# Optimization experiments

Hardware: AMD Instinct MI355X
Metric: run time of the kernel (lower is better)

The kernel has to match this reference:

```python
import jax, jax.numpy as jnp
import numpy as np

B, S, T, H, E, V = 64, 128, 64, 512, 256, 10000


def setup_inputs() -> dict:
    key = jax.random.key(0)
    ks = jax.random.split(key, 16)
    w = 0.05
    return {
        "trg": jax.random.randint(ks[0], (B, T), 0, V),
        "encoder_hidden": jax.random.normal(ks[1], (B, S, 2 * H), jnp.float32),
        "src_lengths": jax.random.randint(ks[2], (B,), 1, S + 1),
        "h0": jax.random.normal(ks[3], (B, H), jnp.float32),
        "c0": jax.random.normal(ks[4], (B, H), jnp.float32),
        "emb_table": jax.random.normal(ks[5], (V, E), jnp.float32) * w,
        "Wkey": jax.random.normal(ks[6], (2 * H, H), jnp.float32) * w,      # attention.key_layer
        "Wquery": jax.random.normal(ks[7], (H, H), jnp.float32) * w,        # attention.query_layer
        "we": jax.random.normal(ks[8], (H,), jnp.float32) * w,              # attention.energy_layer
        "W_ih": jax.random.normal(ks[9], (4 * H, E + 2 * H), jnp.float32) * w,
        "W_hh": jax.random.normal(ks[10], (4 * H, H), jnp.float32) * w,
        "b_ih": jnp.zeros((4 * H,), jnp.float32),
        "b_hh": jnp.zeros((4 * H,), jnp.float32),
        "Wpre": jax.random.normal(ks[11], (3 * H + E, H), jnp.float32) * w,  # pre_output_layer (no bias)
        "Wgen": jax.random.normal(ks[12], (H, V), jnp.float32) * w,          # generator / softmax head
    }


def reference(trg, encoder_hidden, src_lengths, h0, c0, emb_table, Wkey, Wquery,
              we, W_ih, W_hh, b_ih, b_hh, Wpre, Wgen):
    # Teacher-forced unroll (teacher_forcing=True branch); dropout in eval mode.
    s = encoder_hidden.shape[1]
    proj_key = encoder_hidden @ Wkey                            # [B,S,H]
    mask = jnp.arange(s)[None, :] < src_lengths[:, None]        # [B,S]
    embs = emb_table[trg]                                       # [B,T,E]

    def step(carry, emb_t):
        h, c = carry                                            # [B,H] each
        q = h @ Wquery                                          # query = last-layer hidden
        e = jnp.einsum('bsh,h->bs', jnp.tanh(q[:, None, :] + proj_key), we)
        a = jax.nn.softmax(jnp.where(mask, e, -1e9), axis=-1)   # masked attention
        ctx = jnp.einsum('bs,bsd->bd', a, encoder_hidden)       # [B,2H]
        x = jnp.concatenate([emb_t, ctx], axis=-1)              # rnn_input
        g = x @ W_ih.T + h @ W_hh.T + b_ih + b_hh
        i_g, f_g, g_g, o_g = jnp.split(g, 4, axis=-1)           # torch LSTM gate order
        c_new = jax.nn.sigmoid(f_g) * c + jax.nn.sigmoid(i_g) * jnp.tanh(g_g)
        h_new = jax.nn.sigmoid(o_g) * jnp.tanh(c_new)
        pre = jnp.concatenate([emb_t, h_new, ctx], axis=-1) @ Wpre
        logp = jax.nn.log_softmax(pre @ Wgen, axis=-1)          # [B,V]
        return (h_new, c_new), logp

    (hf, cf), out = jax.lax.scan(step, (h0, c0), jnp.swapaxes(embs, 0, 1))
    return jnp.transpose(out, (1, 2, 0)), hf, cf                # out: [B,V,T]
```

## Files before the change

### kernel.cpp

```cpp
#include <hip/hip_runtime.h>

#define B 64
#define S 128
#define T 64
#define H 512
#define E 256
#define V 10000
#define H2 1024
#define G4 2048
#define KX 1536
#define KP 1792
#define VP 10112
#define NROW 4096

typedef unsigned short u16;
typedef __attribute__((ext_vector_type(8))) short bf16x8;
typedef __attribute__((ext_vector_type(4))) short bf16x4;
typedef __attribute__((ext_vector_type(4))) float floatx4;

__device__ inline float b2f(u16 h){
  union { unsigned int u; float f; } v; v.u = ((unsigned int)h) << 16; return v.f;
}
__device__ inline u16 f2b(float f){
  union { unsigned int u; float f; } v; v.f = f;
// ... 156 lines not shown
    *(bf16x8*)&sA[ar*32 + ((ch ^ swz)*8)] = pa;
    #pragma unroll
    for (int i=0;i<NB;i++)
      *(bf16x8*)&sB[(i*64+ar)*32 + ((ch ^ swz)*8)] = pb[i];
    __syncthreads();
    if (k0 + 32 < K){
      pa = *(const bf16x8*)(gA + k0 + 32);
      #pragma unroll
      for (int i=0;i<NB;i++) pb[i] = *(const bf16x8*)(BT + (size_t)(n0+i*64+ar)*ldb + k0+32 + ch*8);
    }
    bf16x8 af = *(const bf16x8*)&sA[(16*wv + (lane&15))*32 + (((lane>>4) ^ px)*8)];
    #pragma unroll
    for (int s=0;s<NSUB;s++){
      bf16x8 bfv = *(const bf16x8*)&sB[(16*s + (lane&15))*32 + (((lane>>4) ^ px)*8)];
      acc[s] = __builtin_amdgcn_mfma_f32_16x16x32_bf16(af, bfv, acc[s], 0, 0, 0);
    }
  }

  if constexpr (EPI == 0 || EPI == 4){
    #pragma unroll
    for (int s=0;s<NSUB;s++)
      #pragma unroll
      for (int r=0;r<4;r++){
        int row = row0 + 16*wv + ((lane>>4)<<2) + r;
        int col = n0 + 16*s + (lane&15);
        if (EPI == 4) row = ((row & 63) << 6) | (row >> 6);
        outb[(size_t)row*ldc + col] = f2b(acc[s][r]);
      }
  }
  if constexpr (EPI == 2){
    float sr[4] = {0.f,0.f,0.f,0.f};
    #pragma unroll
    for (int s=0;s<NSUB;s++){
      int col = n0 + 16*s + (lane&15);
      if (col < V){
        #pragma unroll
        for (int r=0;r<4;r++) sr[r] += __expf(acc[s][r]);
      }
    }
    #pragma unroll
    for (int r=0;r<4;r++){
      float v = sr[r];
      v += __shfl_xor(v,1); v += __shfl_xor(v,2); v += __shfl_xor(v,4); v += __shfl_xor(v,8);
      sr[r] = v;
    }
    if ((lane&15)==0){
      #pragma unroll
      for (int r=0;r<4;r++){
        int row = row0 + 16*wv + ((lane>>4)<<2) + r;
        sep[(size_t)row*80 + blockIdx.y] = sr[r];
      }
    }
  }
  if constexpr (EPI == 3){
    #pragma unroll
    for (int s=0;s<NSUB;s++)
      #pragma unroll
      for (int r=0;r<4;r++){
        int rl = 16*wv + ((lane>>4)<<2) + r;
        int cl = 16*s + (lane&15);
        Cx[cl*65 + rl] = acc[s][r];
      }
    if (tid < 64) lseb[tid] = lse[row0 + tid];
    __syncthreads();
    int b = blockIdx.x;
    for (int idx = tid; idx < TN*16; idx += 256){
      int vl = idx >> 4, q4 = idx & 15;
      int v = n0 + vl;
      if (v < V){
        floatx4 o;
        o[0] = Cx[vl*65 + q4*4+0] - lseb[q4*4+0];
        o[1] = Cx[vl*65 + q4*4+1] - lseb[q4*4+1];
        o[2] = Cx[vl*65 + q4*4+2] - lseb[q4*4+2];
        o[3] = Cx[vl*65 + q4*4+3] - lseb[q4*4+3];
        *(floatx4*)&outp[((size_t)b*V + v)*T + q4*4] = o;
      }
    }
  }
}

__device__ __forceinline__ void wait_flags(unsigned* base, unsigned g){
  if (threadIdx.x < 64){
    unsigned* p = base + (unsigned)threadIdx.x*64;
    int it = 0;
    while (ld_if(p) < g && ++it < 5000000) asm volatile("s_sleep 1":::);
  }
  __syncthreads();
}

__global__ __launch_bounds__(512) void decoder_loop(
    u16* __restrict__ xgs, const float* __restrict__ c0f, float* __restrict__ outp,
    const u16* __restrict__ pk, const u16* __restrict__ encbT,
    const float* __restrict__ we, const int* __restrict__ lens,
    const u16* __restrict__ wqT, u16* __restrict__ cph,
    const u16* __restrict__ wch, const u16* __restrict__ gembt,
    const float* __restrict__ bias, unsigned* __restrict__ bar)
{
  __shared__ u16 sA[64*128];
  __shared__ u16 sB[32*128];
  __shared__ float Cx[64*36];
  __shared__ __align__(16) u16 hsb[H];
  __shared__ __align__(16) float qw[H];
  __shared__ __align__(16) float wel[H];
  __shared__ float ep[512];
  __shared__ float ev[S];
  __shared__ __align__(16) u16 alb[S];
  __shared__ __align__(16) float ctxf[H2];
  __shared__ float smax, sinv;

  const int tid = threadIdx.x, lane = tid & 63, wv = tid >> 6;
  const int blk = blockIdx.x;
  const int b = blk;
  const int lenb = lens[b];
  unsigned* flag_ctx = bar;
  unsigned* flag_h   = bar + 64*64;

  const int n0 = blk*32;
  const int kh = wv >> 2, wr = wv & 3;
  const int rs0 = tid >> 4, gs = tid & 15;
  const int rowa = 16*wr + (lane & 15);
  const int pb_ = tid >> 3, jl = tid & 7;
  const int jglob = n0/4 + jl;
  float creg = c0f[pb_*H + jglob];
  floatx4 bias4 = *(const floatx4*)(bias + n0 + jl*4);

  wel[tid] = we[tid];
  __syncthreads();

  for (int t=0; t<T; t++){
    u16* xgt = xgs + (size_t)t*B*KX;
    u16* xgn = xgs + (size_t)(t+1)*B*KX;

    wait_flags(flag_h, (unsigned)t);
    hsb[tid] = xgt[b*KX + H2 + tid];
    __syncthreads();

    {
      floatx4 accq[4];
      #pragma unroll
      for (int s=0;s<4;s++) accq[s] = (floatx4){0.f,0.f,0.f,0.f};
      const int kc = (lane>>4)*8;
      #pragma unroll 4
      for (int ks=0; ks<16; ks++){
        bf16x8 af = *(const bf16x8*)&hsb[ks*32 + kc];
        #pragma unroll
        for (int s=0;s<4;s++){
          const u16* bp = wqT + (size_t)(wv*64 + s*16 + (lane&15))*H + ks*32 + kc;
          accq[s] = __builtin_amdgcn_mfma_f32_16x16x32_bf16(af, *(const bf16x8*)bp, accq[s], 0, 0, 0);
        }
      }
      if (lane < 16){
        #pragma unroll
        for (int s=0;s<4;s++) qw[wv*64 + s*16 + lane] = accq[s][0];
      }
    }
    __syncthreads();

    {
      int s = tid >> 2, part = tid & 3;
      float a0 = 0.f;
      if (s < lenb){
        const u16* pr = pk + (size_t)(b*S + s)*H;
        #pragma unroll 4
        for (int m=0;m<16;m++){
          int k0 = part*8 + m*32;
          bf16x8 p8 = *(const bf16x8*)(pr + k0);
          floatx4 qa = *(const floatx4*)&qw[k0];
          floatx4 qb = *(const floatx4*)&qw[k0+4];
          floatx4 wa = *(const floatx4*)&wel[k0];
          floatx4 wb = *(const floatx4*)&wel[k0+4];
          #pragma unroll
          for (int i=0;i<4;i++){
            a0 += tanh_fast(qa[i] + b2f((u16)p8[i]))   * wa[i];
            a0 += tanh_fast(qb[i] + b2f((u16)p8[i+4])) * wb[i];
          }
        }
      }
      ep[tid] = a0;
    }
    __syncthreads();
    if (tid < S){
      float e = ep[tid*4] + ep[tid*4+1] + ep[tid*4+2] + ep[tid*4+3];
      ev[tid] = (tid < lenb) ? e : -1e30f;
    }
    __syncthreads();
    if (tid < 64){
      float m = fmaxf(ev[tid], ev[tid+64]);
      #pragma unroll
      for (int o=32;o>=1;o>>=1) m = fmaxf(m, __shfl_xor(m,o));
      if (tid==0) smax = m;
    }
    __syncthreads();
    if (tid < S) ev[tid] = __expf(ev[tid]-smax);
    __syncthreads();
    if (tid < 64){
      float s2 = ev[tid] + ev[tid+64];
      #pragma unroll
      for (int o=32;o>=1;o>>=1) s2 += __shfl_xor(s2,o);
      if (tid==0) sinv = rcpf(s2);
    }
    __syncthreads();
    if (tid < S) alb[tid] = f2b(ev[tid]*sinv);
    __syncthreads();

    {
      floatx4 accc[8];
      #pragma unroll
      for (int s=0;s<8;s++) accc[s] = (floatx4){0.f,0.f,0.f,0.f};
      const int kc = (lane>>4)*8;
      #pragma unroll
      for (int ks=0; ks<4; ks++){
        bf16x8 af = *(const bf16x8*)&alb[ks*32 + kc];
        #pragma unroll
        for (int s8=0;s8<8;s8++){
          const u16* bp = encbT + ((size_t)b*H2 + wv*128 + s8*16 + (lane&15))*S + ks*32 + kc;
          accc[s8] = __builtin_amdgcn_mfma_f32_16x16x32_bf16(af, *(const bf16x8*)bp, accc[s8], 0, 0, 0);
        }
      }
      if (lane < 16){
        #pragma unroll
        for (int s8=0;s8<8;s8++) ctxf[wv*128 + s8*16 + lane] = accc[s8][0];
      }
    }
    __syncthreads();
    {
      int d = tid*2;
      unsigned pack = ((unsigned)f2b(ctxf[d+1]) << 16) | (unsigned)f2b(ctxf[d]);
      st_wt_u32(xgt + (size_t)b*KX + d, pack);
      *(unsigned*)&cph[(size_t)(b*T + t)*KP + E + H + d] = pack;
    }
    asm volatile("s_waitcnt vmcnt(0)" ::: "memory");
    __syncthreads();
    if (tid == 0) st_if(flag_ctx + (unsigned)b*64, (unsigned)(t+1));

    floatx4 gacc[2];
    gacc[0] = (floatx4){0.f,0.f,0.f,0.f};
    gacc[1] = (floatx4){0.f,0.f,0.f,0.f};
    {
      bf16x8 a0 = *(const bf16x8*)(xgt + (size_t)rs0*KX + 1024 + gs*8);
      bf16x8 a1 = *(const bf16x8*)(xgt + (size_t)(rs0+32)*KX + 1024 + gs*8);
      bf16x8 b0 = *(const bf16x8*)(wch + (size_t)(n0+rs0)*KX + 1024 + gs*8);
      for (int kk=8; kk<12; kk++){
        __syncthreads();
        *(bf16x8*)&sA[rs0*128 + ((gs ^ (rs0&7))*8)] = a0;
        *(bf16x8*)&sA[(rs0+32)*128 + ((gs ^ (rs0&7))*8)] = a1;
        *(bf16x8*)&sB[rs0*128 + ((gs ^ (rs0&7))*8)] = b0;
        __syncthreads();
        if (kk < 11){
          int ko = (kk+1)*128;
          a0 = *(const bf16x8*)(xgt + (size_t)rs0*KX + ko + gs*8);
          a1 = *(const bf16x8*)(xgt + (size_t)(rs0+32)*KX + ko + gs*8);
          b0 = *(const bf16x8*)(wch + (size_t)(n0+rs0)*KX + ko + gs*8);
        }
        #pragma unroll
        for (int ks=0; ks<2; ks++){
          int gq = kh*8 + ks*4 + (lane>>4);
          bf16x8 af = *(const bf16x8*)&sA[rowa*128 + ((gq ^ (rowa&7))*8)];
          #pragma unroll
          for (int s=0;s<2;s++){
            int rowb = 16*s + (lane & 15);
            bf16x8 bfv = *(const bf16x8*)&sB[rowb*128 + ((gq ^ (rowb&7))*8)];
            gacc[s] = __builtin_amdgcn_mfma_f32_16x16x32_bf16(af, bfv, gacc[s], 0, 0, 0);
          }
        }
      }
    }

    wait_flags(flag_ctx, (unsigned)(t+1));
    {
      bf16x8 a0 = *(const bf16x8*)(xgt + (size_t)rs0*KX + gs*8);
      bf16x8 a1 = *(const bf16x8*)(xgt + (size_t)(rs0+32)*KX + gs*8);
      bf16x8 b0 = *(const bf16x8*)(wch + (size_t)(n0+rs0)*KX + gs*8);
      for (int kk=0; kk<8; kk++){
        __syncthreads();
        *(bf16x8*)&sA[rs0*128 + ((gs ^ (rs0&7))*8)] = a0;
        *(bf16x8*)&sA[(rs0+32)*128 + ((gs ^ (rs0&7))*8)] = a1;
        *(bf16x8*)&sB[rs0*128 + ((gs ^ (rs0&7))*8)] = b0;
        __syncthreads();
        if (kk < 7){
          int ko = (kk+1)*128;
          a0 = *(const bf16x8*)(xgt + (size_t)rs0*KX + ko + gs*8);
          a1 = *(const bf16x8*)(xgt + (size_t)(rs0+32)*KX + ko + gs*8);
          b0 = *(const bf16x8*)(wch + (size_t)(n0+rs0)*KX + ko + gs*8);
        }
        #pragma unroll
        for (int ks=0; ks<2; ks++){
          int gq = kh*8 + ks*4 + (lane>>4);
          bf16x8 af = *(const bf16x8*)&sA[rowa*128 + ((gq ^ (rowa&7))*8)];
          #pragma unroll
          for (int s=0;s<2;s++){
            int rowb = 16*s + (lane & 15);
            bf16x8 bfv = *(const bf16x8*)&sB[rowb*128 + ((gq ^ (rowb&7))*8)];
            gacc[s] = __builtin_amdgcn_mfma_f32_16x16x32_bf16(af, bfv, gacc[s], 0, 0, 0);
          }
        }
      }
    }
    {
      int r0 = 16*wr + ((lane>>4)<<2);
      if (kh == 1){
        #pragma unroll
        for (int s=0;s<2;s++)
          #pragma unroll
          for (int r=0;r<4;r++) Cx[(r0+r)*36 + 16*s + (lane&15)] = gacc[s][r];
      }
    }
    __syncthreads();
    {
      int r0 = 16*wr + ((lane>>4)<<2);
      if (kh == 0){
        #pragma unroll
        for (int s=0;s<2;s++)
          #pragma unroll
          for (int r=0;r<4;r++) Cx[(r0+r)*36 + 16*s + (lane&15)] += gacc[s][r];
      }
    }
    __syncthreads();
    {
      bf16x4 g4 = *(const bf16x4*)(gembt + (size_t)(t*B + pb_)*G4 + n0 + jl*4);
      float gi = Cx[pb_*36 + jl*4+0] + b2f((u16)g4[0]) + bias4[0];
      float gf = Cx[pb_*36 + jl*4+1] + b2f((u16)g4[1]) + bias4[1];
      float gg = Cx[pb_*36 + jl*4+2] + b2f((u16)g4[2]) + bias4[2];
      float go = Cx[pb_*36 + jl*4+3] + b2f((u16)g4[3]) + bias4[3];
      float cn = sigf(gf)*creg + sigf(gi)*tanh_fast(gg);
      float hn = sigf(go)*tanh_fast(cn);
      creg = cn;
      u16 hb = f2b(hn);
      st_wt_u16(xgn + (size_t)pb_*KX + H2 + jglob, (unsigned)hb);
      cph[(size_t)(pb_*T + t)*KP + E + jglob] = hb;
      if (t == T-1){
        outp[(size_t)B*V*T + pb_*H + jglob] = hn;
        outp[(size_t)B*V*T + B*H + pb_*H + jglob] = cn;
      }
    }
    asm volatile("s_waitcnt vmcnt(0)" ::: "memory");
    __syncthreads();
    if (tid == 0) st_if(flag_h + (unsigned)blk*64, (unsigned)(t+1));
    __syncthreads();
  }
}

static inline int cdiv(int a, int b){ return (a + b - 1) / b; }

extern "C" void kernel_launch(void* const* d_in, const int* in_sizes, int n_in,
                              void* d_out, int out_size, void* d_ws, size_t ws_size,
                              hipStream_t stream)
{
  (void)in_sizes; (void)n_in; (void)out_size; (void)ws_size;
  const int*   trg  = (const int*)d_in[0];
  const float* enc  = (const float*)d_in[1];
  const int*   lens = (const int*)d_in[2];
  const float* h0   = (const float*)d_in[3];
  const float* c0   = (const float*)d_in[4];
  const float* embt = (const float*)d_in[5];
  const float* wkey = (const float*)d_in[6];
  const float* wqry = (const float*)d_in[7];
  const float* we   = (const float*)d_in[8];
  const float* wih  = (const float*)d_in[9];
  const float* whh  = (const float*)d_in[10];
  const float* bi   = (const float*)d_in[11];
  const float* bh   = (const float*)d_in[12];
  const float* wpre = (const float*)d_in[13];
  const float* wgen = (const float*)d_in[14];
  float* out = (float*)d_out;

  char* p = (char*)d_ws;
  auto carve = [&](size_t bytes)->char*{ char* r = p; p += (bytes + 255) & ~(size_t)255; return r; };
  u16*   encb  = (u16*)  carve((size_t)B*S*H2*2);
  u16*   encbT = (u16*)  carve((size_t)B*H2*S*2);
  u16*   pkb   = (u16*)  carve((size_t)B*S*H*2);
  u16*   catp  = (u16*)  carve((size_t)NROW*KP*2);
  u16*   gembb = (u16*)  carve((size_t)NROW*G4*2);
  u16*   preb  = (u16*)  carve((size_t)NROW*H*2);
  u16*   wgt   = (u16*)  carve((size_t)VP*H*2);
  u16*   wch   = (u16*)  carve((size_t)G4*KX*2);
  u16*   wihe  = (u16*)  carve((size_t)G4*E*2);
  u16*   wkeyT = (u16*)  carve((size_t)H*H2*2);
  u16*   wqT   = (u16*)  carve((size_t)H*H*2);
  u16*   wpreT = (u16*)  carve((size_t)H*KP*2);
  u16*   xgs   = (u16*)  carve((size_t)(T+1)*B*KX*2);
  float* biasp = (float*)carve((size_t)G4*4);
  float* sep   = (float*)carve((size_t)NROW*80*4);
  float* lse   = (float*)carve((size_t)NROW*4);
  unsigned* bar = (unsigned*)carve(BAR_WORDS*4);

  k_cast<<<cdiv(B*S*H2,256),256,0,stream>>>(enc, encb, B*S*H2);
  k_encT<<<dim3(H2/64, S/64, B),256,0,stream>>>(enc, encbT);
  k_tct<<<dim3(H/64, H/64),256,0,stream>>>(wqry, wqT, H, H);
  k_tct<<<dim3(H/64, H2/64),256,0,stream>>>(wkey, wkeyT, H2, H);
  k_tct<<<dim3(H/64, KP/64),256,0,stream>>>(wpre, wpreT, KP, H);
  k_tct<<<dim3(VP/64, H/64),256,0,stream>>>(wgen, wgt, H, V);
  k_wch<<<cdiv(G4*KX,256),256,0,stream>>>(wih, whh, wch);
  k_wihe<<<cdiv(G4*E,256),256,0,stream>>>(wih, wihe);
  k_bias<<<cdiv(G4,256),256,0,stream>>>(bi, bh, biasp);
  k_emb<<<cdiv(NROW*E,256),256,0,stream>>>(trg, embt, catp);
  k_init<<<cdiv(B*H,256),256,0,stream>>>(h0, xgs);
  k_zero<<<cdiv(BAR_WORDS,256),256,0,stream>>>(bar);

  gemm_bf16<64,0><<<dim3(B*S/64, H/64),256,0,stream>>>(
      encb, H2, wkeyT, H2, H2, pkb, H, nullptr, nullptr, nullptr);
  gemm_bf16<64,4><<<dim3(NROW/64, G4/64),256,0,stream>>>(
      catp, KP, wihe, E, E, gembb, G4, nullptr, nullptr, nullptr);

  decoder_loop<<<64,512,0,stream>>>(xgs, c0, out, pkb, encbT, we, lens,
                                    wqT, catp, wch, gembb, biasp, bar);

  gemm_bf16<64,0><<<dim3(NROW/64, H/64),256,0,stream>>>(
      catp, KP, wpreT, KP, KP, preb, H, nullptr, nullptr, nullptr);

  gemm_bf16<128,2><<<dim3(NROW/64, VP/128),256,0,stream>>>(
      preb, H, wgt, H, H, nullptr, 0, sep, nullptr, nullptr);
  k_lse<<<cdiv(NROW,256),256,0,stream>>>(sep, lse);
  gemm_bf16<128,3><<<dim3(NROW/64, VP/128),256,0,stream>>>(
      preb, H, wgt, H, H, nullptr, 0, nullptr, out, lse);
}
```

Before: 3.092 ms.

## Split persistent decoder into attention and LSTM-gate block roles with XCD-aware mapping

The persistent decoder kernel now launches 128 blocks instead of 64. Half of them compute attention and context per batch row, and the other half compute the LSTM gate GEMM slices. The two halves synchronise through the existing ctx/h flags, and block IDs are mapped so that cooperating blocks land on the same XCD. The gate blocks prefetch all weight and h-part operands into registers before waiting on the ctx flag. The context MFMA loop also skips K-chunks beyond the source length. The aim is to overlap the attention and gate phases and shorten the serial per-step chain, at the cost of higher register pressure and more co-resident blocks that must all stay live for the spin-wait barriers.

```diff
diff --git a/kernel.cpp b/kernel.cpp
--- a/kernel.cpp
+++ b/kernel.cpp
@@ -290,148 +290,165 @@
 
   const int tid = threadIdx.x, lane = tid & 63, wv = tid >> 6;
   const int blk = blockIdx.x;
-  const int b = blk;
-  const int lenb = lens[b];
+  const int xcd = blk & 7, slot = blk >> 3;
   unsigned* flag_ctx = bar;
   unsigned* flag_h   = bar + 64*64;
 
-  const int n0 = blk*32;
-  const int kh = wv >> 2, wr = wv & 3;
-  const int rs0 = tid >> 4, gs = tid & 15;
-  const int rowa = 16*wr + (lane & 15);
-  const int pb_ = tid >> 3, jl = tid & 7;
-  const int jglob = n0/4 + jl;
-  float creg = c0f[pb_*H + jglob];
-  floatx4 bias4 = *(const floatx4*)(bias + n0 + jl*4);
-
-  wel[tid] = we[tid];
-  __syncthreads();
-
-  for (int t=0; t<T; t++){
-    u16* xgt = xgs + (size_t)t*B*KX;
-    u16* xgn = xgs + (size_t)(t+1)*B*KX;
-
-    wait_flags(flag_h, (unsigned)t);
-    hsb[tid] = xgt[b*KX + H2 + tid];
+  if (slot < 8){
+    const int b = xcd*8 + slot;
+    const int lenb = lens[b];
+    const int nks = (lenb + 31) >> 5;
+    wel[tid] = we[tid];
     __syncthreads();
 
-    {
-      floatx4 accq[4];
-      #pragma unroll
-      for (int s=0;s<4;s++) accq[s] = (floatx4){0.f,0.f,0.f,0.f};
-      const int kc = (lane>>4)*8;
-      #pragma unroll 4
-      for (int ks=0; ks<16; ks++){
-        bf16x8 af = *(const bf16x8*)&hsb[ks*32 + kc];
+    for (int t=0; t<T; t++){
+      wait_flags(flag_h, (unsigned)t);
+      u16* xgt = xgs + (size_t)t*B*KX;
+      hsb[tid] = xgt[b*KX + H2 + tid];
+      __syncthreads();
+      {
+        floatx4 accq[4];
         #pragma unroll
-        for (int s=0;s<4;s++){
-          const u16* bp = wqT + (size_t)(wv*64 + s*16 + (lane&15))*H + ks*32 + kc;
-          accq[s] = __builtin_amdgcn_mfma_f32_16x16x32_bf16(af, *(const bf16x8*)bp, accq[s], 0, 0, 0);
-        }
-      }
-      if (lane < 16){
+        for (int s=0;s<4;s++) accq[s] = (floatx4){0.f,0.f,0.f,0.f};
+        const int kc = (lane>>4)*8;
+        #pragma unroll 4
+        for (int ks=0; ks<16; ks++){
+          bf16x8 af = *(const bf16x8*)&hsb[ks*32 + kc];
+          #pragma unroll
+          for (int s=0;s<4;s++){
+            const u16* bp = wqT + (size_t)(wv*64 + s*16 + (lane&15))*H + ks*32 + kc;
+            accq[s] = __builtin_amdgcn_mfma_f32_16x16x32_bf16(af, *(const bf16x8*)bp, accq[s], 0, 0, 0);
+          }
+        }
+        if (lane < 16){
+          #pragma unroll
+          for (int s=0;s<4;s++) qw[wv*64 + s*16 + lane] = accq[s][0];
+        }
+      }
+      __syncthreads();
+      {
+        int s = tid >> 2, part = tid & 3;
+        float a0 = 0.f;
+        if (s < lenb){
+          const u16* pr = pk + (size_t)(b*S + s)*H;
+          #pragma unroll 4
+          for (int m=0;m<16;m++){
+            int k0 = part*8 + m*32;
+            bf16x8 p8 = *(const bf16x8*)(pr + k0);
+            floatx4 qa = *(const floatx4*)&qw[k0];
+            floatx4 qb = *(const floatx4*)&qw[k0+4];
+            floatx4 wa = *(const floatx4*)&wel[k0];
+            floatx4 wb = *(const floatx4*)&wel[k0+4];
+            #pragma unroll
+            for (int i=0;i<4;i++){
+              a0 += tanh_fast(qa[i] + b2f((u16)p8[i]))   * wa[i];
+              a0 += tanh_fast(qb[i] + b2f((u16)p8[i+4])) * wb[i];
+            }
+          }
+        }
+        ep[tid] = a0;
+      }
+      __syncthreads();
+      if (tid < S){
+        float e = ep[tid*4] + ep[tid*4+1] + ep[tid*4+2] + ep[tid*4+3];
+        ev[tid] = (tid < lenb) ? e : -1e30f;
+      }
+      __syncthreads();
+      if (tid < 64){
+        float m = fmaxf(ev[tid], ev[tid+64]);
         #pragma unroll
-        for (int s=0;s<4;s++) qw[wv*64 + s*16 + lane] = accq[s][0];
-      }
-    }
-    __syncthreads();
-
-    {
-      int s = tid >> 2, part = tid & 3;
-      float a0 = 0.f;
-      if (s < lenb){
-        const u16* pr = pk + (size_t)(b*S + s)*H;
-        #pragma unroll 4
-        for (int m=0;m<16;m++){
-          int k0 = part*8 + m*32;
-          bf16x8 p8 = *(const bf16x8*)(pr + k0);
-          floatx4 qa = *(const floatx4*)&qw[k0];
-          floatx4 qb = *(const floatx4*)&qw[k0+4];
-          floatx4 wa = *(const floatx4*)&wel[k0];
-          floatx4 wb = *(const floatx4*)&wel[k0+4];
-          #pragma unroll
-          for (int i=0;i<4;i++){
-            a0 += tanh_fast(qa[i] + b2f((u16)p8[i]))   * wa[i];
-            a0 += tanh_fast(qb[i] + b2f((u16)p8[i+4])) * wb[i];
+        for (int o=32;o>=1;o>>=1) m = fmaxf(m, __shfl_xor(m,o));
+        if (tid==0) smax = m;
+      }
+      __syncthreads();
+      if (tid < S) ev[tid] = __expf(ev[tid]-smax);
+      __syncthreads();
+      if (tid < 64){
+        float s2 = ev[tid] + ev[tid+64];
+        #pragma unroll
+        for (int o=32;o>=1;o>>=1) s2 += __shfl_xor(s2,o);
+        if (tid==0) sinv = rcpf(s2);
+      }
+      __syncthreads();
+      if (tid < S) alb[tid] = f2b(ev[tid]*sinv);
+      __syncthreads();
+      {
+        floatx4 accc[8];
+        #pragma unroll
+        for (int s=0;s<8;s++) accc[s] = (floatx4){0.f,0.f,0.f,0.f};
+        const int kc = (lane>>4)*8;
+        for (int ks=0; ks<nks; ks++){
+          bf16x8 af = *(const bf16x8*)&alb[ks*32 + kc];
+          #pragma unroll
+          for (int s8=0;s8<8;s8++){
+            const u16* bp = encbT + ((size_t)b*H2 + wv*128 + s8*16 + (lane&15))*S + ks*32 + kc;
+            accc[s8] = __builtin_amdgcn_mfma_f32_16x16x32_bf16(af, *(const bf16x8*)bp, accc[s8], 0, 0, 0);
           }
         }
-      }
-      ep[tid] = a0;
-    }
-    __syncthreads();
-    if (tid < S){
-      float e = ep[tid*4] + ep[tid*4+1] + ep[tid*4+2] + ep[tid*4+3];
-      ev[tid] = (tid < lenb) ? e : -1e30f;
-    }
-    __syncthreads();
-    if (tid < 64){
-      float m = fmaxf(ev[tid], ev[tid+64]);
-      #pragma unroll
-      for (int o=32;o>=1;o>>=1) m = fmaxf(m, __shfl_xor(m,o));
-      if (tid==0) smax = m;
-    }
-    __syncthreads();
-    if (tid < S) ev[tid] = __expf(ev[tid]-smax);
-    __syncthreads();
-    if (tid < 64){
-      float s2 = ev[tid] + ev[tid+64];
-      #pragma unroll
-      for (int o=32;o>=1;o>>=1) s2 += __shfl_xor(s2,o);
-      if (tid==0) sinv = rcpf(s2);
-    }
-    __syncthreads();
-    if (tid < S) alb[tid] = f2b(ev[tid]*sinv);
-    __syncthreads();
-
-    {
-      floatx4 accc[8];
-      #pragma unroll
-      for (int s=0;s<8;s++) accc[s] = (floatx4){0.f,0.f,0.f,0.f};
-      const int kc = (lane>>4)*8;
-      #pragma unroll
-      for (int ks=0; ks<4; ks++){
-        bf16x8 af = *(const bf16x8*)&alb[ks*32 + kc];
-        #pragma unroll
-        for (int s8=0;s8<8;s8++){
-          const u16* bp = encbT + ((size_t)b*H2 + wv*128 + s8*16 + (lane&15))*S + ks*32 + kc;
-          accc[s8] = __builtin_amdgcn_mfma_f32_16x16x32_bf16(af, *(const bf16x8*)bp, accc[s8], 0, 0, 0);
-        }
-      }
-      if (lane < 16){
-        #pragma unroll
-        for (int s8=0;s8<8;s8++) ctxf[wv*128 + s8*16 + lane] = accc[s8][0];
-      }
-    }
-    __syncthreads();
-    {
-      int d = tid*2;
-      unsigned pack = ((unsigned)f2b(ctxf[d+1]) << 16) | (unsigned)f2b(ctxf[d]);
-      st_wt_u32(xgt + (size_t)b*KX + d, pack);
-      *(unsigned*)&cph[(size_t)(b*T + t)*KP + E + H + d] = pack;
-    }
-    asm volatile("s_waitcnt vmcnt(0)" ::: "memory");
-    __syncthreads();
-    if (tid == 0) st_if(flag_ctx + (unsigned)b*64, (unsigned)(t+1));
-
-    floatx4 gacc[2];
-    gacc[0] = (floatx4){0.f,0.f,0.f,0.f};
-    gacc[1] = (floatx4){0.f,0.f,0.f,0.f};
-    {
-      bf16x8 a0 = *(const bf16x8*)(xgt + (size_t)rs0*KX + 1024 + gs*8);
-      bf16x8 a1 = *(const bf16x8*)(xgt + (size_t)(rs0+32)*KX + 1024 + gs*8);
-      bf16x8 b0 = *(const bf16x8*)(wch + (size_t)(n0+rs0)*KX + 1024 + gs*8);
-      for (int kk=8; kk<12; kk++){
+        if (lane < 16){
+          #pragma unroll
+          for (int s8=0;s8<8;s8++) ctxf[wv*128 + s8*16 + lane] = accc[s8][0];
+        }
+      }
+      __syncthreads();
+      {
+        int d = tid*2;
+        unsigned pack = ((unsigned)f2b(ctxf[d+1]) << 16) | (unsigned)f2b(ctxf[d]);
+        st_wt_u32(xgt + (size_t)b*KX + d, pack);
+        *(unsigned*)&cph[(size_t)(b*T + t)*KP + E + H + d] = pack;
+      }
+      asm volatile("s_waitcnt vmcnt(0)" ::: "memory");
+      __syncthreads();
+      if (tid == 0) st_if(flag_ctx + (unsigned)b*64, (unsigned)(t+1));
+      __syncthreads();
+    }
+  } else {
+    const int g = slot - 8;
+    const int gid = xcd*8 + g;
+    const int n0 = xcd*256 + g*32;
+    const int kh = wv >> 2, wr = wv & 3;
+    const int rs0 = tid >> 4, gs = tid & 15;
+    const int rowa = 16*wr + (lane & 15);
+    const int pb_ = tid >> 3, jl = tid & 7;
+    const int jglob = n0/4 + jl;
+    float creg = c0f[pb_*H + jglob];
+    floatx4 bias4 = *(const floatx4*)(bias + n0 + jl*4);
+
+    for (int t=0; t<T; t++){
+      const u16* xgt = xgs + (size_t)t*B*KX;
+      u16* xgn = xgs + (size_t)(t+1)*B*KX;
+
+      bf16x4 g4 = *(const bf16x4*)(gembt + (size_t)(t*B + pb_)*G4 + n0 + jl*4);
+      bf16x8 pbv[12];
+      #pragma unroll
+      for (int kk=0; kk<12; kk++)
+        pbv[kk] = *(const bf16x8*)(wch + (size_t)(n0+rs0)*KX + kk*128 + gs*8);
+      bf16x8 ph0[4], ph1[4];
+      #pragma unroll
+      for (int m=0; m<4; m++){
+        ph0[m] = *(const bf16x8*)(xgt + (size_t)rs0*KX + (8+m)*128 + gs*8);
+        ph1[m] = *(const bf16x8*)(xgt + (size_t)(rs0+32)*KX + (8+m)*128 + gs*8);
+      }
+
+      wait_flags(flag_ctx, (unsigned)(t+1));
+      bf16x8 pc0[8], pc1[8];
+      #pragma unroll
+      for (int m=0; m<8; m++){
+        pc0[m] = *(const bf16x8*)(xgt + (size_t)rs0*KX + m*128 + gs*8);
+        pc1[m] = *(const bf16x8*)(xgt + (size_t)(rs0+32)*KX + m*128 + gs*8);
+      }
+
+      floatx4 gacc[2];
+      gacc[0] = (floatx4){0.f,0.f,0.f,0.f};
+      gacc[1] = (floatx4){0.f,0.f,0.f,0.f};
+
+      #pragma unroll
+      for (int m=0; m<4; m++){
         __syncthreads();
-        *(bf16x8*)&sA[rs0*128 + ((gs ^ (rs0&7))*8)] = a0;
-        *(bf16x8*)&sA[(rs0+32)*128 + ((gs ^ (rs0&7))*8)] = a1;
-        *(bf16x8*)&sB[rs0*128 + ((gs ^ (rs0&7))*8)] = b0;
+        *(bf16x8*)&sA[rs0*128 + ((gs ^ (rs0&7))*8)] = ph0[m];
+        *(bf16x8*)&sA[(rs0+32)*128 + ((gs ^ (rs0&7))*8)] = ph1[m];
+        *(bf16x8*)&sB[rs0*128 + ((gs ^ (rs0&7))*8)] = pbv[8+m];
         __syncthreads();
-        if (kk < 11){
-          int ko = (kk+1)*128;
-          a0 = *(const bf16x8*)(xgt + (size_t)rs0*KX + ko + gs*8);
-          a1 = *(const bf16x8*)(xgt + (size_t)(rs0+32)*KX + ko + gs*8);
-          b0 = *(const bf16x8*)(wch + (size_t)(n0+rs0)*KX + ko + gs*8);
-        }
         #pragma unroll
         for (int ks=0; ks<2; ks++){
           int gq = kh*8 + ks*4 + (lane>>4);
@@ -444,25 +461,13 @@
           }
         }
       }
-    }
-
-    wait_flags(flag_ctx, (unsigned)(t+1));
-    {
-      bf16x8 a0 = *(const bf16x8*)(xgt + (size_t)rs0*KX + gs*8);
-      bf16x8 a1 = *(const bf16x8*)(xgt + (size_t)(rs0+32)*KX + gs*8);
-      bf16x8 b0 = *(const bf16x8*)(wch + (size_t)(n0+rs0)*KX + gs*8);
-      for (int kk=0; kk<8; kk++){
+      #pragma unroll
+      for (int m=0; m<8; m++){
         __syncthreads();
-        *(bf16x8*)&sA[rs0*128 + ((gs ^ (rs0&7))*8)] = a0;
-        *(bf16x8*)&sA[(rs0+32)*128 + ((gs ^ (rs0&7))*8)] = a1;
-        *(bf16x8*)&sB[rs0*128 + ((gs ^ (rs0&7))*8)] = b0;
+        *(bf16x8*)&sA[rs0*128 + ((gs ^ (rs0&7))*8)] = pc0[m];
+        *(bf16x8*)&sA[(rs0+32)*128 + ((gs ^ (rs0&7))*8)] = pc1[m];
+        *(bf16x8*)&sB[rs0*128 + ((gs ^ (rs0&7))*8)] = pbv[m];
         __syncthreads();
-        if (kk < 7){
-          int ko = (kk+1)*128;
-          a0 = *(const bf16x8*)(xgt + (size_t)rs0*KX + ko + gs*8);
-          a1 = *(const bf16x8*)(xgt + (size_t)(rs0+32)*KX + ko + gs*8);
-          b0 = *(const bf16x8*)(wch + (size_t)(n0+rs0)*KX + ko + gs*8);
-        }
         #pragma unroll
         for (int ks=0; ks<2; ks++){
           int gq = kh*8 + ks*4 + (lane>>4);
@@ -475,48 +480,47 @@
           }
         }
       }
-    }
-    {
-      int r0 = 16*wr + ((lane>>4)<<2);
-      if (kh == 1){
-        #pragma unroll
-        for (int s=0;s<2;s++)
-          #pragma unroll
-          for (int r=0;r<4;r++) Cx[(r0+r)*36 + 16*s + (lane&15)] = gacc[s][r];
-      }
-    }
-    __syncthreads();
-    {
-      int r0 = 16*wr + ((lane>>4)<<2);
-      if (kh == 0){
-        #pragma unroll
-        for (int s=0;s<2;s++)
-          #pragma unroll
-          for (int r=0;r<4;r++) Cx[(r0+r)*36 + 16*s + (lane&15)] += gacc[s][r];
-      }
-    }
-    __syncthreads();
-    {
-      bf16x4 g4 = *(const bf16x4*)(gembt + (size_t)(t*B + pb_)*G4 + n0 + jl*4);
-      float gi = Cx[pb_*36 + jl*4+0] + b2f((u16)g4[0]) + bias4[0];
-      float gf = Cx[pb_*36 + jl*4+1] + b2f((u16)g4[1]) + bias4[1];
-      float gg = Cx[pb_*36 + jl*4+2] + b2f((u16)g4[2]) + bias4[2];
-      float go = Cx[pb_*36 + jl*4+3] + b2f((u16)g4[3]) + bias4[3];
-      float cn = sigf(gf)*creg + sigf(gi)*tanh_fast(gg);
-      float hn = sigf(go)*tanh_fast(cn);
-      creg = cn;
-      u16 hb = f2b(hn);
-      st_wt_u16(xgn + (size_t)pb_*KX + H2 + jglob, (unsigned)hb);
-      cph[(size_t)(pb_*T + t)*KP + E + jglob] = hb;
-      if (t == T-1){
-        outp[(size_t)B*V*T + pb_*H + jglob] = hn;
-        outp[(size_t)B*V*T + B*H + pb_*H + jglob] = cn;
-      }
-    }
-    asm volatile("s_waitcnt vmcnt(0)" ::: "memory");
-    __syncthreads();
-    if (tid == 0) st_if(flag_h + (unsigned)blk*64, (unsigned)(t+1));
-    __syncthreads();
+      {
+        int r0 = 16*wr + ((lane>>4)<<2);
+        if (kh == 1){
+          #pragma unroll
+          for (int s=0;s<2;s++)
+            #pragma unroll
+            for (int r=0;r<4;r++) Cx[(r0+r)*36 + 16*s + (lane&15)] = gacc[s][r];
+        }
+      }
+      __syncthreads();
+      {
+        int r0 = 16*wr + ((lane>>4)<<2);
+        if (kh == 0){
+          #pragma unroll
+          for (int s=0;s<2;s++)
+            #pragma unroll
+            for (int r=0;r<4;r++) Cx[(r0+r)*36 + 16*s + (lane&15)] += gacc[s][r];
+        }
+      }
+      __syncthreads();
+      {
+        float gi = Cx[pb_*36 + jl*4+0] + b2f((u16)g4[0]) + bias4[0];
+        float gf = Cx[pb_*36 + jl*4+1] + b2f((u16)g4[1]) + bias4[1];
+        float gg = Cx[pb_*36 + jl*4+2] + b2f((u16)g4[2]) + bias4[2];
+        float go = Cx[pb_*36 + jl*4+3] + b2f((u16)g4[3]) + bias4[3];
+        float cn = sigf(gf)*creg + sigf(gi)*tanh_fast(gg);
+        float hn = sigf(go)*tanh_fast(cn);
+        creg = cn;
+        u16 hb = f2b(hn);
+        st_wt_u16(xgn + (size_t)pb_*KX + H2 + jglob, (unsigned)hb);
+        cph[(size_t)(pb_*T + t)*KP + E + jglob] = hb;
+        if (t == T-1){
+          outp[(size_t)B*V*T + pb_*H + jglob] = hn;
+          outp[(size_t)B*V*T + B*H + pb_*H + jglob] = cn;
+        }
+      }
+      asm volatile("s_waitcnt vmcnt(0)" ::: "memory");
+      __syncthreads();
+      if (tid == 0) st_if(flag_h + (unsigned)gid*64, (unsigned)(t+1));
+      __syncthreads();
+    }
   }
 }
 
@@ -582,8 +586,8 @@
   gemm_bf16<64,4><<<dim3(NROW/64, G4/64),256,0,stream>>>(
       catp, KP, wihe, E, E, gembb, G4, nullptr, nullptr, nullptr);
 
-  decoder_loop<<<64,512,0,stream>>>(xgs, c0, out, pkb, encbT, we, lens,
-                                    wqT, catp, wch, gembb, biasp, bar);
+  decoder_loop<<<128,512,0,stream>>>(xgs, c0, out, pkb, encbT, we, lens,
+                                     wqT, catp, wch, gembb, biasp, bar);
 
   gemm_bf16<64,0><<<dim3(NROW/64, H/64),256,0,stream>>>(
       catp, KP, wpreT, KP, KP, preb, H, nullptr, nullptr, nullptr);
```

Result: faster. 2.589 ms (-16.3%).

## Split persistent decoder into attention and LSTM-gate blocks with LDS-resident weights

Applied to the files above, without the earlier changes.

The persistent decoder launches 128 blocks instead of 64. The first 64 handle attention and context for one batch row each. The other 64 handle the LSTM gate GEMM, keeping their 32-row slice of the combined weight resident in shared memory, and the blocks are mapped so that related blocks share an XCD. The context GEMM now skips key chunks beyond the source length, the softmax is folded into a single wave, and the A tile is double-buffered. Spin waits check the flag once before sleeping longer. In exchange the kernel needs about 140KB of LDS per block and all 128 blocks must be co-resident for the flag handshake to work.

```diff
diff --git a/kernel.cpp b/kernel.cpp
--- a/kernel.cpp
+++ b/kernel.cpp
@@ -262,8 +262,10 @@
 __device__ __forceinline__ void wait_flags(unsigned* base, unsigned g){
   if (threadIdx.x < 64){
     unsigned* p = base + (unsigned)threadIdx.x*64;
-    int it = 0;
-    while (ld_if(p) < g && ++it < 5000000) asm volatile("s_sleep 1":::);
+    if (ld_if(p) < g){
+      int it = 0;
+      do { asm volatile("s_sleep 8":::); } while (ld_if(p) < g && ++it < 1000000);
+    }
   }
   __syncthreads();
 }
@@ -276,247 +278,255 @@
     const u16* __restrict__ wch, const u16* __restrict__ gembt,
     const float* __restrict__ bias, unsigned* __restrict__ bar)
 {
-  __shared__ u16 sA[64*128];
-  __shared__ u16 sB[32*128];
-  __shared__ float Cx[64*36];
-  __shared__ __align__(16) u16 hsb[H];
-  __shared__ __align__(16) float qw[H];
-  __shared__ __align__(16) float wel[H];
-  __shared__ float ep[512];
-  __shared__ float ev[S];
-  __shared__ __align__(16) u16 alb[S];
-  __shared__ __align__(16) float ctxf[H2];
-  __shared__ float smax, sinv;
+  __shared__ char pool[140288];
 
   const int tid = threadIdx.x, lane = tid & 63, wv = tid >> 6;
   const int blk = blockIdx.x;
-  const int b = blk;
-  const int lenb = lens[b];
+  const int xcd = blk & 7, slot = blk >> 3;
   unsigned* flag_ctx = bar;
   unsigned* flag_h   = bar + 64*64;
 
-  const int n0 = blk*32;
-  const int kh = wv >> 2, wr = wv & 3;
-  const int rs0 = tid >> 4, gs = tid & 15;
-  const int rowa = 16*wr + (lane & 15);
-  const int pb_ = tid >> 3, jl = tid & 7;
-  const int jglob = n0/4 + jl;
-  float creg = c0f[pb_*H + jglob];
-  floatx4 bias4 = *(const floatx4*)(bias + n0 + jl*4);
-
-  wel[tid] = we[tid];
-  __syncthreads();
-
-  for (int t=0; t<T; t++){
-    u16* xgt = xgs + (size_t)t*B*KX;
-    u16* xgn = xgs + (size_t)(t+1)*B*KX;
-
-    wait_flags(flag_h, (unsigned)t);
-    hsb[tid] = xgt[b*KX + H2 + tid];
+  if (slot < 8){
+    u16*   hsb  = (u16*)pool;
+    float* qw   = (float*)(pool + 1024);
+    float* wel  = (float*)(pool + 3072);
+    float* ep   = (float*)(pool + 5120);
+    float* ev   = (float*)(pool + 7168);
+    u16*   alb  = (u16*)(pool + 7680);
+    float* ctxf = (float*)(pool + 8192);
+
+    const int b = xcd*8 + slot;
+    const int lenb = lens[b];
+    const int nks = (lenb + 31) >> 5;
+    wel[tid] = we[tid];
     __syncthreads();
 
-    {
-      floatx4 accq[4];
-      #pragma unroll
-      for (int s=0;s<4;s++) accq[s] = (floatx4){0.f,0.f,0.f,0.f};
-      const int kc = (lane>>4)*8;
-      #pragma unroll 4
-      for (int ks=0; ks<16; ks++){
-        bf16x8 af = *(const bf16x8*)&hsb[ks*32 + kc];
+    for (int t=0; t<T; t++){
+      wait_flags(flag_h, (unsigned)t);
+      u16* xgt = xgs + (size_t)t*B*KX;
+      hsb[tid] = xgt[b*KX + H2 + tid];
+      __syncthreads();
+      {
+        floatx4 accq[4];
         #pragma unroll
-        for (int s=0;s<4;s++){
-          const u16* bp = wqT + (size_t)(wv*64 + s*16 + (lane&15))*H + ks*32 + kc;
-          accq[s] = __builtin_amdgcn_mfma_f32_16x16x32_bf16(af, *(const bf16x8*)bp, accq[s], 0, 0, 0);
-        }
-      }
-      if (lane < 16){
+        for (int s=0;s<4;s++) accq[s] = (floatx4){0.f,0.f,0.f,0.f};
+        const int kc = (lane>>4)*8;
+        #pragma unroll 4
+        for (int ks=0; ks<16; ks++){
+          bf16x8 af = *(const bf16x8*)&hsb[ks*32 + kc];
+          #pragma unroll
+          for (int s=0;s<4;s++){
+            const u16* bp = wqT + (size_t)(wv*64 + s*16 + (lane&15))*H + ks*32 + kc;
+            accq[s] = __builtin_amdgcn_mfma_f32_16x16x32_bf16(af, *(const bf16x8*)bp, accq[s], 0, 0, 0);
+          }
+        }
+        if (lane < 16){
+          #pragma unroll
+          for (int s=0;s<4;s++) qw[wv*64 + s*16 + lane] = accq[s][0];
+        }
+      }
+      __syncthreads();
+      {
+        int s = tid >> 2, part = tid & 3;
+        float a0 = 0.f;
+        if (s < lenb){
+          const u16* pr = pk + (size_t)(b*S + s)*H;
+          #pragma unroll 4
+          for (int m=0;m<16;m++){
+            int k0 = part*8 + m*32;
+            bf16x8 p8 = *(const bf16x8*)(pr + k0);
+            floatx4 qa = *(const floatx4*)&qw[k0];
+            floatx4 qb = *(const floatx4*)&qw[k0+4];
+            floatx4 wa = *(const floatx4*)&wel[k0];
+            floatx4 wb = *(const floatx4*)&wel[k0+4];
+            #pragma unroll
+            for (int i=0;i<4;i++){
+              a0 += tanh_fast(qa[i] + b2f((u16)p8[i]))   * wa[i];
+              a0 += tanh_fast(qb[i] + b2f((u16)p8[i+4])) * wb[i];
+            }
+          }
+        }
+        ep[tid] = a0;
+      }
+      __syncthreads();
+      if (wv == 0){
+        int s0 = lane, s1 = lane + 64;
+        float e0 = ep[s0*4]+ep[s0*4+1]+ep[s0*4+2]+ep[s0*4+3];
+        float e1 = ep[s1*4]+ep[s1*4+1]+ep[s1*4+2]+ep[s1*4+3];
+        bool m0 = s0 < lenb, m1 = s1 < lenb;
+        float mx = fmaxf(m0 ? e0 : -1e30f, m1 ? e1 : -1e30f);
         #pragma unroll
-        for (int s=0;s<4;s++) qw[wv*64 + s*16 + lane] = accq[s][0];
-      }
+        for (int o=32;o>=1;o>>=1) mx = fmaxf(mx, __shfl_xor(mx,o));
+        float p0 = m0 ? __expf(e0-mx) : 0.f;
+        float p1 = m1 ? __expf(e1-mx) : 0.f;
+        float sm = p0 + p1;
+        #pragma unroll
+        for (int o=32;o>=1;o>>=1) sm += __shfl_xor(sm,o);
+        float sinv = rcpf(sm);
+        alb[s0] = f2b(p0*sinv);
+        alb[s1] = f2b(p1*sinv);
+      }
+      __syncthreads();
+      {
+        floatx4 accc[8];
+        #pragma unroll
+        for (int s=0;s<8;s++) accc[s] = (floatx4){0.f,0.f,0.f,0.f};
+        const int kc = (lane>>4)*8;
+        for (int ks=0; ks<nks; ks++){
+          bf16x8 af = *(const bf16x8*)&alb[ks*32 + kc];
+          #pragma unroll
+          for (int s8=0;s8<8;s8++){
+            const u16* bp = encbT + ((size_t)b*H2 + wv*128 + s8*16 + (lane&15))*S + ks*32 + kc;
+            accc[s8] = __builtin_amdgcn_mfma_f32_16x16x32_bf16(af, *(const bf16x8*)bp, accc[s8], 0, 0, 0);
+          }
+        }
+        if (lane < 16){
+          #pragma unroll
+          for (int s8=0;s8<8;s8++) ctxf[wv*128 + s8*16 + lane] = accc[s8][0];
+        }
+      }
+      __syncthreads();
+      {
+        int d = tid*2;
+        unsigned pack = ((unsigned)f2b(ctxf[d+1]) << 16) | (unsigned)f2b(ctxf[d]);
+        st_wt_u32(xgt + (size_t)b*KX + d, pack);
+        *(unsigned*)&cph[(size_t)(b*T + t)*KP + E + H + d] = pack;
+      }
+      asm volatile("s_waitcnt vmcnt(0)" ::: "memory");
+      __syncthreads();
+      if (tid == 0) st_if(flag_ctx + (unsigned)b*64, (unsigned)(t+1));
+      __syncthreads();
+    }
+  } else {
+    u16*   sB  = (u16*)pool;
+    u16*   sA0 = (u16*)(pool + 98304);
+    u16*   sA1 = (u16*)(pool + 114688);
+    float* Cx  = (float*)(pool + 131072);
+
+    const int g = slot - 8;
+    const int gid = xcd*8 + g;
+    const int n0 = xcd*256 + g*32;
+    const int kh = wv >> 2, wr = wv & 3;
+    const int rs0 = tid >> 4, gs = tid & 15;
+    const int rowa = 16*wr + (lane & 15);
+    const int pb_ = tid >> 3, jl = tid & 7;
+    const int jglob = n0/4 + jl;
+    float creg = c0f[pb_*H + jglob];
+    floatx4 bias4 = *(const floatx4*)(bias + n0 + jl*4);
+
+    for (int u = tid; u < 32*192; u += 512){
+      int row = u / 192, cl = u % 192;
+      int kk = cl >> 4, c = cl & 15;
+      *(bf16x8*)&sB[row*1536 + kk*128 + ((c ^ (row&7))*8)] =
+          *(const bf16x8*)(wch + (size_t)(n0+row)*KX + kk*128 + c*8);
     }
     __syncthreads();
 
-    {
-      int s = tid >> 2, part = tid & 3;
-      float a0 = 0.f;
-      if (s < lenb){
-        const u16* pr = pk + (size_t)(b*S + s)*H;
-        #pragma unroll 4
-        for (int m=0;m<16;m++){
-          int k0 = part*8 + m*32;
-          bf16x8 p8 = *(const bf16x8*)(pr + k0);
-          floatx4 qa = *(const floatx4*)&qw[k0];
-          floatx4 qb = *(const floatx4*)&qw[k0+4];
-          floatx4 wa = *(const floatx4*)&wel[k0];
-          floatx4 wb = *(const floatx4*)&wel[k0+4];
-          #pragma unroll
-          for (int i=0;i<4;i++){
-            a0 += tanh_fast(qa[i] + b2f((u16)p8[i]))   * wa[i];
-            a0 += tanh_fast(qb[i] + b2f((u16)p8[i+4])) * wb[i];
+    for (int t=0; t<T; t++){
+      const u16* xgt = xgs + (size_t)t*B*KX;
+      u16* xgn = xgs + (size_t)(t+1)*B*KX;
+      bf16x4 g4 = *(const bf16x4*)(gembt + (size_t)(t*B + pb_)*G4 + n0 + jl*4);
+
+      floatx4 gacc[2];
+      gacc[0] = (floatx4){0.f,0.f,0.f,0.f};
+      gacc[1] = (floatx4){0.f,0.f,0.f,0.f};
+
+      {
+        bf16x8 a0 = *(const bf16x8*)(xgt + (size_t)rs0*KX + 8*128 + gs*8);
+        bf16x8 a1 = *(const bf16x8*)(xgt + (size_t)(rs0+32)*KX + 8*128 + gs*8);
+        for (int kk=8; kk<12; kk++){
+          u16* sAc = (kk & 1) ? sA1 : sA0;
+          *(bf16x8*)&sAc[rs0*128 + ((gs ^ (rs0&7))*8)] = a0;
+          *(bf16x8*)&sAc[(rs0+32)*128 + ((gs ^ (rs0&7))*8)] = a1;
+          __syncthreads();
+          if (kk < 11){
+            int ko = (kk+1)*128;
+            a0 = *(const bf16x8*)(xgt + (size_t)rs0*KX + ko + gs*8);
+            a1 = *(const bf16x8*)(xgt + (size_t)(rs0+32)*KX + ko + gs*8);
           }
-        }
-      }
-      ep[tid] = a0;
-    }
-    __syncthreads();
-    if (tid < S){
-      float e = ep[tid*4] + ep[tid*4+1] + ep[tid*4+2] + ep[tid*4+3];
-      ev[tid] = (tid < lenb) ? e : -1e30f;
-    }
-    __syncthreads();
-    if (tid < 64){
-      float m = fmaxf(ev[tid], ev[tid+64]);
-      #pragma unroll
-      for (int o=32;o>=1;o>>=1) m = fmaxf(m, __shfl_xor(m,o));
-      if (tid==0) smax = m;
-    }
-    __syncthreads();
-    if (tid < S) ev[tid] = __expf(ev[tid]-smax);
-    __syncthreads();
-    if (tid < 64){
-      float s2 = ev[tid] + ev[tid+64];
-      #pragma unroll
-      for (int o=32;o>=1;o>>=1) s2 += __shfl_xor(s2,o);
-      if (tid==0) sinv = rcpf(s2);
-    }
-    __syncthreads();
-    if (tid < S) alb[tid] = f2b(ev[tid]*sinv);
-    __syncthreads();
-
-    {
-      floatx4 accc[8];
-      #pragma unroll
-      for (int s=0;s<8;s++) accc[s] = (floatx4){0.f,0.f,0.f,0.f};
-      const int kc = (lane>>4)*8;
-      #pragma unroll
-      for (int ks=0; ks<4; ks++){
-        bf16x8 af = *(const bf16x8*)&alb[ks*32 + kc];
-        #pragma unroll
-        for (int s8=0;s8<8;s8++){
-          const u16* bp = encbT + ((size_t)b*H2 + wv*128 + s8*16 + (lane&15))*S + ks*32 + kc;
-          accc[s8] = __builtin_amdgcn_mfma_f32_16x16x32_bf16(af, *(const bf16x8*)bp, accc[s8], 0, 0, 0);
-        }
-      }
-      if (lane < 16){
-        #pragma unroll
-        for (int s8=0;s8<8;s8++) ctxf[wv*128 + s8*16 + lane] = accc[s8][0];
-      }
-    }
-    __syncthreads();
-    {
-      int d = tid*2;
-      unsigned pack = ((unsigned)f2b(ctxf[d+1]) << 16) | (unsigned)f2b(ctxf[d]);
-      st_wt_u32(xgt + (size_t)b*KX + d, pack);
-      *(unsigned*)&cph[(size_t)(b*T + t)*KP + E + H + d] = pack;
-    }
-    asm volatile("s_waitcnt vmcnt(0)" ::: "memory");
-    __syncthreads();
-    if (tid == 0) st_if(flag_ctx + (unsigned)b*64, (unsigned)(t+1));
-
-    floatx4 gacc[2];
-    gacc[0] = (floatx4){0.f,0.f,0.f,0.f};
-    gacc[1] = (floatx4){0.f,0.f,0.f,0.f};
-    {
-      bf16x8 a0 = *(const bf16x8*)(xgt + (size_t)rs0*KX + 1024 + gs*8);
-      bf16x8 a1 = *(const bf16x8*)(xgt + (size_t)(rs0+32)*KX + 1024 + gs*8);
-      bf16x8 b0 = *(const bf16x8*)(wch + (size_t)(n0+rs0)*KX + 1024 + gs*8);
-      for (int kk=8; kk<12; kk++){
-        __syncthreads();
-        *(bf16x8*)&sA[rs0*128 + ((gs ^ (rs0&7))*8)] = a0;
-        *(bf16x8*)&sA[(rs0+32)*128 + ((gs ^ (rs0&7))*8)] = a1;
-        *(bf16x8*)&sB[rs0*128 + ((gs ^ (rs0&7))*8)] = b0;
-        __syncthreads();
-        if (kk < 11){
-          int ko = (kk+1)*128;
-          a0 = *(const bf16x8*)(xgt + (size_t)rs0*KX + ko + gs*8);
-          a1 = *(const bf16x8*)(xgt + (size_t)(rs0+32)*KX + ko + gs*8);
-          b0 = *(const bf16x8*)(wch + (size_t)(n0+rs0)*KX + ko + gs*8);
-        }
-        #pragma unroll
-        for (int ks=0; ks<2; ks++){
-          int gq = kh*8 + ks*4 + (lane>>4);
-          bf16x8 af = *(const bf16x8*)&sA[rowa*128 + ((gq ^ (rowa&7))*8)];
-          #pragma unroll
-          for (int s=0;s<2;s++){
-            int rowb = 16*s + (lane & 15);
-            bf16x8 bfv = *(const bf16x8*)&sB[rowb*128 + ((gq ^ (rowb&7))*8)];
-            gacc[s] = __builtin_amdgcn_mfma_f32_16x16x32_bf16(af, bfv, gacc[s], 0, 0, 0);
+          #pragma unroll
+          for (int ks=0; ks<2; ks++){
+            int gq = kh*8 + ks*4 + (lane>>4);
+            bf16x8 af = *(const bf16x8*)&sAc[rowa*128 + ((gq ^ (rowa&7))*8)];
+            #pragma unroll
+            for (int s=0;s<2;s++){
+              int rowb = 16*s + (lane & 15);
+              bf16x8 bfv = *(const bf16x8*)&sB[rowb*1536 + kk*128 + ((gq ^ (rowb&7))*8)];
+              gacc[s] = __builtin_amdgcn_mfma_f32_16x16x32_bf16(af, bfv, gacc[s], 0, 0, 0);
+            }
           }
-        }
-      }
-    }
-
-    wait_flags(flag_ctx, (unsigned)(t+1));
-    {
-      bf16x8 a0 = *(const bf16x8*)(xgt + (size_t)rs0*KX + gs*8);
-      bf16x8 a1 = *(const bf16x8*)(xgt + (size_t)(rs0+32)*KX + gs*8);
-      bf16x8 b0 = *(const bf16x8*)(wch + (size_t)(n0+rs0)*KX + gs*8);
-      for (int kk=0; kk<8; kk++){
-        __syncthreads();
-        *(bf16x8*)&sA[rs0*128 + ((gs ^ (rs0&7))*8)] = a0;
-        *(bf16x8*)&sA[(rs0+32)*128 + ((gs ^ (rs0&7))*8)] = a1;
-        *(bf16x8*)&sB[rs0*128 + ((gs ^ (rs0&7))*8)] = b0;
-        __syncthreads();
-        if (kk < 7){
-          int ko = (kk+1)*128;
-          a0 = *(const bf16x8*)(xgt + (size_t)rs0*KX + ko + gs*8);
-          a1 = *(const bf16x8*)(xgt + (size_t)(rs0+32)*KX + ko + gs*8);
-          b0 = *(const bf16x8*)(wch + (size_t)(n0+rs0)*KX + ko + gs*8);
-        }
-        #pragma unroll
-        for (int ks=0; ks<2; ks++){
-          int gq = kh*8 + ks*4 + (lane>>4);
-          bf16x8 af = *(const bf16x8*)&sA[rowa*128 + ((gq ^ (rowa&7))*8)];
-          #pragma unroll
-          for (int s=0;s<2;s++){
-            int rowb = 16*s + (lane & 15);
-            bf16x8 bfv = *(const bf16x8*)&sB[rowb*128 + ((gq ^ (rowb&7))*8)];
-            gacc[s] = __builtin_amdgcn_mfma_f32_16x16x32_bf16(af, bfv, gacc[s], 0, 0, 0);
+          __syncthreads();
+        }
+      }
+      wait_flags(flag_ctx, (unsigned)(t+1));
+      {
+        bf16x8 a0 = *(const bf16x8*)(xgt + (size_t)rs0*KX + gs*8);
+        bf16x8 a1 = *(const bf16x8*)(xgt + (size_t)(rs0+32)*KX + gs*8);
+        for (int kk=0; kk<8; kk++){
+          u16* sAc = (kk & 1) ? sA1 : sA0;
+          *(bf16x8*)&sAc[rs0*128 + ((gs ^ (rs0&7))*8)] = a0;
+          *(bf16x8*)&sAc[(rs0+32)*128 + ((gs ^ (rs0&7))*8)] = a1;
+          __syncthreads();
+          if (kk < 7){
+            int ko = (kk+1)*128;
+            a0 = *(const bf16x8*)(xgt + (size_t)rs0*KX + ko + gs*8);
+            a1 = *(const bf16x8*)(xgt + (size_t)(rs0+32)*KX + ko + gs*8);
           }
-        }
-      }
-    }
-    {
-      int r0 = 16*wr + ((lane>>4)<<2);
-      if (kh == 1){
-        #pragma unroll
-        for (int s=0;s<2;s++)
-          #pragma unroll
-          for (int r=0;r<4;r++) Cx[(r0+r)*36 + 16*s + (lane&15)] = gacc[s][r];
-      }
-    }
-    __syncthreads();
-    {
-      int r0 = 16*wr + ((lane>>4)<<2);
-      if (kh == 0){
-        #pragma unroll
-        for (int s=0;s<2;s++)
-          #pragma unroll
-          for (int r=0;r<4;r++) Cx[(r0+r)*36 + 16*s + (lane&15)] += gacc[s][r];
-      }
-    }
-    __syncthreads();
-    {
-      bf16x4 g4 = *(const bf16x4*)(gembt + (size_t)(t*B + pb_)*G4 + n0 + jl*4);
-      float gi = Cx[pb_*36 + jl*4+0] + b2f((u16)g4[0]) + bias4[0];
-      float gf = Cx[pb_*36 + jl*4+1] + b2f((u16)g4[1]) + bias4[1];
-      float gg = Cx[pb_*36 + jl*4+2] + b2f((u16)g4[2]) + bias4[2];
-      float go = Cx[pb_*36 + jl*4+3] + b2f((u16)g4[3]) + bias4[3];
-      float cn = sigf(gf)*creg + sigf(gi)*tanh_fast(gg);
-      float hn = sigf(go)*tanh_fast(cn);
-      creg = cn;
-      u16 hb = f2b(hn);
-      st_wt_u16(xgn + (size_t)pb_*KX + H2 + jglob, (unsigned)hb);
-      cph[(size_t)(pb_*T + t)*KP + E + jglob] = hb;
-      if (t == T-1){
-        outp[(size_t)B*V*T + pb_*H + jglob] = hn;
-        outp[(size_t)B*V*T + B*H + pb_*H + jglob] = cn;
-      }
-    }
-    asm volatile("s_waitcnt vmcnt(0)" ::: "memory");
-    __syncthreads();
-    if (tid == 0) st_if(flag_h + (unsigned)blk*64, (unsigned)(t+1));
-    __syncthreads();
+          #pragma unroll
+          for (int ks=0; ks<2; ks++){
+            int gq = kh*8 + ks*4 + (lane>>4);
+            bf16x8 af = *(const bf16x8*)&sAc[rowa*128 + ((gq ^ (rowa&7))*8)];
+            #pragma unroll
+            for (int s=0;s<2;s++){
+              int rowb = 16*s + (lane & 15);
+              bf16x8 bfv = *(const bf16x8*)&sB[rowb*1536 + kk*128 + ((gq ^ (rowb&7))*8)];
+              gacc[s] = __builtin_amdgcn_mfma_f32_16x16x32_bf16(af, bfv, gacc[s], 0, 0, 0);
+            }
+          }
+          __syncthreads();
+        }
+      }
+      {
+        int r0 = 16*wr + ((lane>>4)<<2);
+        if (kh == 1){
+          #pragma unroll
+          for (int s=0;s<2;s++)
+            #pragma unroll
+            for (int r=0;r<4;r++) Cx[(r0+r)*36 + 16*s + (lane&15)] = gacc[s][r];
+        }
+      }
+      __syncthreads();
+      {
+        int r0 = 16*wr + ((lane>>4)<<2);
+        if (kh == 0){
+          #pragma unroll
+          for (int s=0;s<2;s++)
+            #pragma unroll
+            for (int r=0;r<4;r++) Cx[(r0+r)*36 + 16*s + (lane&15)] += gacc[s][r];
+        }
+      }
+      __syncthreads();
+      {
+        float gi = Cx[pb_*36 + jl*4+0] + b2f((u16)g4[0]) + bias4[0];
+        float gf = Cx[pb_*36 + jl*4+1] + b2f((u16)g4[1]) + bias4[1];
+        float gg = Cx[pb_*36 + jl*4+2] + b2f((u16)g4[2]) + bias4[2];
+        float go = Cx[pb_*36 + jl*4+3] + b2f((u16)g4[3]) + bias4[3];
+        float cn = sigf(gf)*creg + sigf(gi)*tanh_fast(gg);
+        float hn = sigf(go)*tanh_fast(cn);
+        creg = cn;
+        u16 hb = f2b(hn);
+        st_wt_u16(xgn + (size_t)pb_*KX + H2 + jglob, (unsigned)hb);
+        cph[(size_t)(pb_*T + t)*KP + E + jglob] = hb;
+        if (t == T-1){
+          outp[(size_t)B*V*T + pb_*H + jglob] = hn;
+          outp[(size_t)B*V*T + B*H + pb_*H + jglob] = cn;
+        }
+      }
+      asm volatile("s_waitcnt vmcnt(0)" ::: "memory");
+      __syncthreads();
+      if (tid == 0) st_if(flag_h + (unsigned)gid*64, (unsigned)(t+1));
+      __syncthreads();
+    }
   }
 }
 
@@ -582,8 +592,8 @@
   gemm_bf16<64,4><<<dim3(NROW/64, G4/64),256,0,stream>>>(
       catp, KP, wihe, E, E, gembb, G4, nullptr, nullptr, nullptr);
 
-  decoder_loop<<<64,512,0,stream>>>(xgs, c0, out, pkb, encbT, we, lens,
-                                    wqT, catp, wch, gembb, biasp, bar);
+  decoder_loop<<<128,512,0,stream>>>(xgs, c0, out, pkb, encbT, we, lens,
+                                     wqT, catp, wch, gembb, biasp, bar);
 
   gemm_bf16<64,0><<<dim3(NROW/64, H/64),256,0,stream>>>(
       catp, KP, wpreT, KP, KP, preb, H, nullptr, nullptr, nullptr);
```

Result: faster. 2.516 ms (-18.6%).
